# Kernel optimization log

Hardware: AMD Instinct MI355X
Metric: run time of the kernel (lower is better)

Reference implementation:

```python
import jax, jax.numpy as jnp
import numpy as np

B, T, D, H = 4, 2048, 1024, 16
HD = D // H  # head_dim = 64
ROPE_BASE = 10000.0


def rotate_half(x):
    # Faithful to source: interleaved rotate. x[..., ::2], x[..., 1::2]
    x1 = x[..., ::2]
    x2 = x[..., 1::2]
    return jnp.stack((-x2, x1), axis=-1).reshape(x.shape)


def rope_tables(seq_len, dim, dtype=jnp.float32):
    inv = 1.0 / (ROPE_BASE ** (jnp.arange(0, dim, 2, dtype=jnp.float32) / dim))
    t = jnp.arange(seq_len, dtype=jnp.float32)
    freqs = jnp.einsum('i,j->ij', t, inv)          # [T, dim/2]
    emb = jnp.concatenate((freqs, freqs), axis=-1)  # [T, dim]
    return jnp.cos(emb).astype(dtype)[None, None], jnp.sin(emb).astype(dtype)[None, None]


def setup_inputs() -> dict:
    key = jax.random.key(0)
    ks = jax.random.split(key, 9)
    s = 0.02
    return {
        'x':  jax.random.normal(ks[0], (B, T, D), jnp.float32),
        'Wq': jax.random.normal(ks[1], (D, D), jnp.float32) * s,
        'bq': jnp.zeros((D,), jnp.float32),
        'Wk': jax.random.normal(ks[2], (D, D), jnp.float32) * s,
        'bk': jnp.zeros((D,), jnp.float32),
        'Wv': jax.random.normal(ks[3], (D, D), jnp.float32) * s,
        'bv': jnp.zeros((D,), jnp.float32),
        'Wo': jax.random.normal(ks[4], (D, D), jnp.float32) * s,
        'bo': jnp.zeros((D,), jnp.float32),
    }


def reference(x, Wq, bq, Wk, bk, Wv, bv, Wo, bo):
    b, t, d = x.shape
    # QKV projections -> [B, H, T, HD]
    def proj(W, bias):
        return (x @ W.T + bias).reshape(b, t, H, HD).transpose(0, 2, 1, 3)
    q, k, v = proj(Wq, bq), proj(Wk, bk), proj(Wv, bv)
    # RoPE (as written in source: non-interleaved cos/sin with interleaved rotate_half)
    cos, sin = rope_tables(t, HD, x.dtype)
    q = q * cos + rotate_half(q) * sin
    k = k * cos + rotate_half(k) * sin
    # Attention
    scale = 1.0 / jnp.sqrt(jnp.asarray(HD, x.dtype))
    attn = jnp.einsum('bhqd,bhkd->bhqk', q, k) * scale
    attn = jax.nn.softmax(attn, axis=-1)
    out = jnp.einsum('bhqk,bhkd->bhqd', attn, v)
    out = out.transpose(0, 2, 1, 3).reshape(b, t, d)
    return out @ Wo.T + bo
```

## Files before the change

### kernel.cpp

```cpp
#include <hip/hip_runtime.h>
#include <hip/hip_bf16.h>

constexpr int Bb = 4, Tt = 2048, Dd = 1024, Hh = 16, HD = 64;
constexpr int Mm = Bb * Tt;

typedef __attribute__((ext_vector_type(8))) short bf16x8;
typedef __attribute__((ext_vector_type(4))) short s16x4;
typedef __attribute__((ext_vector_type(4))) float f32x4;
typedef __attribute__((ext_vector_type(16))) float f32x16;

__device__ __forceinline__ short f2bf(float f) {
  union { float f; unsigned u; } v; v.f = f;
  unsigned r = (v.u + 0x7fffu + ((v.u >> 16) & 1u)) >> 16;
  return (short)r;
}

__device__ __forceinline__ unsigned cvt_pk_bf16(float lo, float hi) {
  unsigned r;
  asm("v_cvt_pk_bf16_f32 %0, %1, %2" : "=v"(r) : "v"(lo), "v"(hi));
  return r;
}

__device__ __forceinline__ void gl_lds16(const short* gsrc, short* ldst) {
  __builtin_amdgcn_global_load_lds(
      (const __attribute__((address_space(1))) void*)gsrc,
      (__attribute__((address_space(3))) void*)ldst, 16, 0, 0);
}

__global__ __launch_bounds__(256) void cvt_k(const float* __restrict__ src,
                                             short* __restrict__ dst, int n4) {
  int i = blockIdx.x * 256 + threadIdx.x;
  if (i >= n4) return;
  float4 v = ((const float4*)src)[i];
  s16x4 p = { f2bf(v.x), f2bf(v.y), f2bf(v.z), f2bf(v.w) };
  ((s16x4*)dst)[i] = p;
}

__global__ void rope_tab(float* __restrict__ cs, float* __restrict__ sn) {
  int idx = blockIdx.x * 256 + threadIdx.x;
  if (idx >= Tt * HD) return;
  int t = idx >> 6, d = idx & (HD - 1);
  float f = powf(10000.0f, -(float)(d & 31) / 32.0f);
  float ang = (float)t * f;
  cs[idx] = cosf(ang);
  sn[idx] = sinf(ang);
}

template<int EPI>
__global__ __launch_bounds__(256) void gemm_fast(
    const short* __restrict__ Ab, const short* __restrict__ Wb,
    const float* __restrict__ bias,
    short* __restrict__ outb, float* __restrict__ outf,
    const float* __restrict__ cs, const float* __restrict__ sn)
{
  constexpr int K = 1024;
  __shared__ short Alds[128 * 64];
  __shared__ short Blds[128 * 64];
  const int tid = threadIdx.x;
  const int lane = tid & 63, wave = tid >> 6;
  const int g = lane >> 4, li = lane & 15;
  const int m0 = blockIdx.x * 128, n0 = blockIdx.y * 128;
  const int wm = (wave >> 1) * 64, wn = (wave & 1) * 64;
  f32x4 acc[4][4] = {};

  const int lrow = lane >> 3;
  const int soff = lrow * K + (((lane & 7) ^ lrow) * 8);
  const short* Asrc = Ab + (size_t)(m0 + wave * 32) * K + soff;
  const short* Bsrc = Wb + (size_t)(n0 + wave * 32) * K + soff;
  short* Adst = Alds + wave * 32 * 64;
  short* Bdst = Blds + wave * 32 * 64;

  for (int k0 = 0; k0 < K; k0 += 64) {
    #pragma unroll
    for (int i = 0; i < 4; i++) {
      gl_lds16(Asrc + (size_t)i * 8 * K + k0, Adst + i * 8 * 64);
      gl_lds16(Bsrc + (size_t)i * 8 * K + k0, Bdst + i * 8 * 64);
    }
    __syncthreads();

    bf16x8 af[4][2], bfr[4][2];
    #pragma unroll
    for (int i = 0; i < 4; i++) {
      int row = wm + i * 16 + li, sw = li & 7;
      #pragma unroll
      for (int kk = 0; kk < 2; kk++)
        af[i][kk] = *(const bf16x8*)&Alds[row * 64 + (((kk * 4 + g) ^ sw) * 8)];
    }
    #pragma unroll
    for (int j = 0; j < 4; j++) {
      int row = wn + j * 16 + li, sw = li & 7;
      #pragma unroll
      for (int kk = 0; kk < 2; kk++)
        bfr[j][kk] = *(const bf16x8*)&Blds[row * 64 + (((kk * 4 + g) ^ sw) * 8)];
    }
    #pragma unroll
    for (int i = 0; i < 4; i++)
      #pragma unroll
      for (int j = 0; j < 4; j++)
        #pragma unroll
        for (int kk = 0; kk < 2; kk++)
          acc[i][j] = __builtin_amdgcn_mfma_f32_16x16x32_bf16(
              af[i][kk], bfr[j][kk], acc[i][j], 0, 0, 0);
    __syncthreads();
  }

  #pragma unroll
  for (int i = 0; i < 4; i++)
    #pragma unroll
    for (int j = 0; j < 4; j++)
      #pragma unroll
      for (int r = 0; r < 4; r++) {
        int m = m0 + wm + i * 16 + g * 4 + r;
        int n = n0 + wn + j * 16 + li;
        float val = acc[i][j][r] + bias[n];
        if constexpr (EPI == 0 || EPI == 1) {
          float partner = __shfl_xor(val, 1, 64);
          int tt = m & (Tt - 1), hd = n & (HD - 1);
          float c = cs[tt * HD + hd], s = sn[tt * HD + hd];
          float rh = (n & 1) ? partner : -partner;
          val = val * c + rh * s;
          if constexpr (EPI == 0) val *= 0.18033688f;
        }
        if constexpr (EPI <= 1) {
          int bI = m >> 11, tt = m & (Tt - 1), h = n >> 6, hd = n & (HD - 1);
          outb[(((size_t)bI * Hh + h) * Tt + tt) * HD + hd] = f2bf(val);
        } else {
          outf[(size_t)m * Dd + n] = val;
        }
      }
}

__global__ __launch_bounds__(256) void gemm_v(
    const short* __restrict__ Ab, const float* __restrict__ Wf,
    const float* __restrict__ bias, short* __restrict__ outb)
{
  constexpr int K = 1024;
  __shared__ short Alds[128][72];
  __shared__ short Blds[128][72];
  const int tid = threadIdx.x;
  const int lane = tid & 63, wave = tid >> 6;
  const int g = lane >> 4, li = lane & 15;
  const int m0 = blockIdx.x * 128, n0 = blockIdx.y * 128;
  const int wm = (wave >> 1) * 64, wn = (wave & 1) * 64;
  f32x4 acc[4][4] = {};

  for (int k0 = 0; k0 < K; k0 += 64) {
    #pragma unroll
    for (int s = 0; s < 4; s++) {
      int f = tid + s * 256; int row = f >> 3, c8 = f & 7;
      *(bf16x8*)&Alds[row][c8 * 8] =
          *(const bf16x8*)(Ab + (size_t)(m0 + row) * K + k0 + c8 * 8);
    }
    #pragma unroll
    for (int s = 0; s < 8; s++) {
      int f = tid + s * 256; int row = f >> 4, c4 = f & 15;
      float4 v = *(const float4*)(Wf + (size_t)(n0 + row) * K + k0 + c4 * 4);
      s16x4 p = { f2bf(v.x), f2bf(v.y), f2bf(v.z), f2bf(v.w) };
      *(s16x4*)&Blds[row][c4 * 4] = p;
    }
    __syncthreads();

    bf16x8 af[4][2], bfr[4][2];
    #pragma unroll
    for (int i = 0; i < 4; i++)
      #pragma unroll
      for (int kk = 0; kk < 2; kk++)
        af[i][kk] = *(const bf16x8*)&Alds[wm + i * 16 + li][kk * 32 + g * 8];
    #pragma unroll
    for (int j = 0; j < 4; j++)
      #pragma unroll
      for (int kk = 0; kk < 2; kk++)
        bfr[j][kk] = *(const bf16x8*)&Blds[wn + j * 16 + li][kk * 32 + g * 8];
    #pragma unroll
    for (int i = 0; i < 4; i++)
      #pragma unroll
      for (int j = 0; j < 4; j++)
        #pragma unroll
        for (int kk = 0; kk < 2; kk++)
          acc[i][j] = __builtin_amdgcn_mfma_f32_16x16x32_bf16(
              af[i][kk], bfr[j][kk], acc[i][j], 0, 0, 0);
    __syncthreads();
  }

  #pragma unroll
  for (int i = 0; i < 4; i++)
    #pragma unroll
    for (int j = 0; j < 4; j++) {
      int n = n0 + wn + j * 16 + li;
      s16x4 pk;
      #pragma unroll
      for (int r = 0; r < 4; r++) pk[r] = f2bf(acc[i][j][r] + bias[n]);
      int mb = m0 + wm + i * 16 + g * 4;
      int bI = mb >> 11, t0 = mb & (Tt - 1), h = n >> 6, d = n & (HD - 1);
      *(s16x4*)(outb + (((size_t)bI * Hh + h) * HD + d) * Tt + t0) = pk;
    }
}

__device__ __forceinline__ void store_o(const f32x16& o, float inv,
                                        short* __restrict__ AO, size_t rowbase,
                                        int colbase, int h) {
  #pragma unroll
  for (int R = 0; R < 4; R++) {
    s16x4 pk;
    #pragma unroll
    for (int j = 0; j < 4; j++) pk[j] = f2bf(o[R * 4 + j] * inv);
    *(s16x4*)(AO + rowbase + colbase + 8 * R + 4 * h) = pk;
  }
}

__global__ __launch_bounds__(128, 4) void attn_k(
    const short* __restrict__ Qb, const short* __restrict__ Kb,
    const short* __restrict__ Vt_g, short* __restrict__ AO)
{
  __shared__ short Klds[64][72];
  __shared__ short Vt[64][72];
  const int tid = threadIdx.x, lane = tid & 63, wave = tid >> 6;
  const int h = lane >> 5;
  const int ql = lane & 31;
  const int bh = blockIdx.x;
  const int q0 = blockIdx.y * 64 + wave * 32;
  const size_t base  = (size_t)bh * Tt * HD;
  const size_t basev = (size_t)bh * HD * Tt;

  bf16x8 qf[4];
  #pragma unroll
  for (int ks = 0; ks < 4; ks++)
    qf[ks] = *(const bf16x8*)(Qb + base + (size_t)(q0 + ql) * HD + ks * 16 + h * 8);

  float m_i = -3.0e38f, l_i = 0.f;
  f32x16 o0 = {}, o1 = {};

  for (int kv0 = 0; kv0 < Tt; kv0 += 64) {
    #pragma unroll
    for (int s = 0; s < 4; s++) {
      int f = tid + s * 128; int row = f >> 3, c8 = f & 7;
      *(bf16x8*)&Klds[row][c8 * 8] =
          *(const bf16x8*)(Kb + base + (size_t)(kv0 + row) * HD + c8 * 8);
      *(bf16x8*)&Vt[row][c8 * 8] =
          *(const bf16x8*)(Vt_g + basev + (size_t)row * Tt + kv0 + c8 * 8);
    }
    __syncthreads();

    f32x16 st0 = {}, st1 = {};
    __builtin_amdgcn_s_setprio(1);
    #pragma unroll
    for (int ks = 0; ks < 4; ks++) {
      bf16x8 kf0 = *(const bf16x8*)&Klds[ql][ks * 16 + h * 8];
      bf16x8 kf1 = *(const bf16x8*)&Klds[32 + ql][ks * 16 + h * 8];
      st0 = __builtin_amdgcn_mfma_f32_32x32x16_bf16(kf0, qf[ks], st0, 0, 0, 0);
      st1 = __builtin_amdgcn_mfma_f32_32x32x16_bf16(kf1, qf[ks], st1, 0, 0, 0);
    }
    __builtin_amdgcn_s_setprio(0);

    float mv = st0[0];
    #pragma unroll
    for (int r = 1; r < 16; r++) mv = fmaxf(mv, st0[r]);
    #pragma unroll
    for (int r = 0; r < 16; r++) mv = fmaxf(mv, st1[r]);
    mv = fmaxf(mv, __shfl_xor(mv, 32, 64));
    float mn = fmaxf(m_i, mv);
    float corr = __builtin_amdgcn_exp2f(m_i - mn);
    m_i = mn;

    float rs = 0.f;
    #pragma unroll
    for (int r = 0; r < 16; r++) { st0[r] = __builtin_amdgcn_exp2f(st0[r] - mn); rs += st0[r]; }
    #pragma unroll
    for (int r = 0; r < 16; r++) { st1[r] = __builtin_amdgcn_exp2f(st1[r] - mn); rs += st1[r]; }
    rs += __shfl_xor(rs, 32, 64);
    l_i = l_i * corr + rs;

    #pragma unroll
    for (int r = 0; r < 16; r++) { o0[r] *= corr; o1[r] *= corr; }

    __builtin_amdgcn_s_setprio(1);
    #pragma unroll
    for (int ks = 0; ks < 4; ks++) {
      const int b0 = ((2 * ks) & 3) * 4;
      float A0, A1, A2, A3, B0, B1, B2, B3;
      if (ks < 2) {
        A0 = st0[b0]; A1 = st0[b0 + 1]; A2 = st0[b0 + 2]; A3 = st0[b0 + 3];
        B0 = st0[b0 + 4]; B1 = st0[b0 + 5]; B2 = st0[b0 + 6]; B3 = st0[b0 + 7];
      } else {
        A0 = st1[b0]; A1 = st1[b0 + 1]; A2 = st1[b0 + 2]; A3 = st1[b0 + 3];
        B0 = st1[b0 + 4]; B1 = st1[b0 + 5]; B2 = st1[b0 + 6]; B3 = st1[b0 + 7];
      }
      unsigned wa0 = cvt_pk_bf16(A0, A1), wa1 = cvt_pk_bf16(A2, A3);
      unsigned wb0 = cvt_pk_bf16(B0, B1), wb1 = cvt_pk_bf16(B2, B3);
      unsigned s0 = h ? wa0 : wb0, s1 = h ? wa1 : wb1;
      unsigned r0 = (unsigned)__shfl_xor((int)s0, 32, 64);
      unsigned r1 = (unsigned)__shfl_xor((int)s1, 32, 64);
      unsigned own0 = h ? wb0 : wa0, own1 = h ? wb1 : wa1;
      union { unsigned u[4]; bf16x8 v; } pa;
      pa.u[0] = h ? r0 : own0;  pa.u[1] = h ? r1 : own1;
      pa.u[2] = h ? own0 : r0;  pa.u[3] = h ? own1 : r1;

      bf16x8 vf0 = *(const bf16x8*)&Vt[ql][ks * 16 + h * 8];
      bf16x8 vf1 = *(const bf16x8*)&Vt[32 + ql][ks * 16 + h * 8];
      o0 = __builtin_amdgcn_mfma_f32_32x32x16_bf16(vf0, pa.v, o0, 0, 0, 0);
      o1 = __builtin_amdgcn_mfma_f32_32x32x16_bf16(vf1, pa.v, o1, 0, 0, 0);
    }
    __builtin_amdgcn_s_setprio(0);
    __syncthreads();
  }

  float inv = 1.0f / l_i;
  const int b = bh >> 4, hh = bh & 15;
  size_t rowbase = ((size_t)b * Tt + q0 + ql) * Dd;
  store_o(o0, inv, AO, rowbase, hh * 64 + 0, h);
  store_o(o1, inv, AO, rowbase, hh * 64 + 32, h);
}

extern "C" void kernel_launch(void* const* d_in, const int* in_sizes, int n_in,
                              void* d_out, int out_size, void* d_ws, size_t ws_size,
                              hipStream_t stream)
{
  const float* x  = (const float*)d_in[0];
  const float* Wq = (const float*)d_in[1];
  const float* bq = (const float*)d_in[2];
  const float* Wk = (const float*)d_in[3];
  const float* bk = (const float*)d_in[4];
  const float* Wv = (const float*)d_in[5];
  const float* bv = (const float*)d_in[6];
  const float* Wo = (const float*)d_in[7];
  const float* bo = (const float*)d_in[8];
  float* out = (float*)d_out;

  char* ws = (char*)d_ws;
  float* cs = (float*)ws;
  float* sn = (float*)(ws + (size_t)(1 << 19));
  char*  p0 = ws + ((size_t)1 << 20);
  short* Qb = (short*)(p0);
  short* Kb = (short*)(p0 + ((size_t)16 << 20));
  short* Vb = (short*)(p0 + ((size_t)32 << 20));
  short* xb = (short*)(p0 + ((size_t)48 << 20));
  short* AO  = xb;
  short* Wqb = Kb;
  short* Wkb = Vb;
  short* Wob = Kb;

  cvt_k<<<dim3(Mm * Dd / 4 / 256), dim3(256), 0, stream>>>(x,  xb,  Mm * Dd / 4);
  cvt_k<<<dim3(Dd * Dd / 4 / 256), dim3(256), 0, stream>>>(Wq, Wqb, Dd * Dd / 4);
  cvt_k<<<dim3(Dd * Dd / 4 / 256), dim3(256), 0, stream>>>(Wk, Wkb, Dd * Dd / 4);
  rope_tab<<<dim3(512), dim3(256), 0, stream>>>(cs, sn);

  dim3 gg(Mm / 128, Dd / 128), bb(256);
  gemm_fast<0><<<gg, bb, 0, stream>>>(xb, Wqb, bq, Qb, nullptr, cs, sn);
  gemm_fast<1><<<gg, bb, 0, stream>>>(xb, Wkb, bk, Kb, nullptr, cs, sn);
  gemm_v<<<gg, bb, 0, stream>>>(xb, Wv, bv, Vb);

  attn_k<<<dim3(Bb * Hh, Tt / 64), dim3(128), 0, stream>>>(Qb, Kb, Vb, AO);

  cvt_k<<<dim3(Dd * Dd / 4 / 256), dim3(256), 0, stream>>>(Wo, Wob, Dd * Dd / 4);
  gemm_fast<3><<<gg, bb, 0, stream>>>(AO, Wob, bo, nullptr, out, cs, sn);
}
```

Measured before the change: 232.6 us.

## Batch Q/K projections into one launch and add lazy softmax rescaling

Merges the Q and K projection GEMMs into a single launch that picks the weight, bias and output by blockIdx.z, moving the weight buffers so both converted weights can live at once. The separate output-projection GEMM kernel is specialised to drop the RoPE epilogue branches. In attention, the row max now uses a v_max3 reduction tree, and the running max and rescale of the output and sum are only updated when the new max exceeds the old one by more than 8 in log2 space. Skipping the rescale removes per-tile multiplies but lets exponentials reach up to 2^8 before normalisation, which slightly changes the numerics.

```diff
diff --git a/kernel.cpp b/kernel.cpp
--- a/kernel.cpp
+++ b/kernel.cpp
@@ -19,6 +19,12 @@
   unsigned r;
   asm("v_cvt_pk_bf16_f32 %0, %1, %2" : "=v"(r) : "v"(lo), "v"(hi));
   return r;
+}
+
+__device__ __forceinline__ float max3f(float a, float b, float c) {
+  float d;
+  asm("v_max3_f32 %0, %1, %2, %3" : "=v"(d) : "v"(a), "v"(b), "v"(c));
+  return d;
 }
 
 __device__ __forceinline__ void gl_lds16(const short* gsrc, short* ldst) {
@@ -46,12 +52,92 @@
   sn[idx] = sinf(ang);
 }
 
-template<int EPI>
-__global__ __launch_bounds__(256) void gemm_fast(
+__global__ __launch_bounds__(256) void gemm_qk(
+    const short* __restrict__ Ab,
+    const short* __restrict__ Wqb, const short* __restrict__ Wkb,
+    const float* __restrict__ bq, const float* __restrict__ bk,
+    short* __restrict__ Qo, short* __restrict__ Ko,
+    const float* __restrict__ cs, const float* __restrict__ sn)
+{
+  constexpr int K = 1024;
+  __shared__ short Alds[128 * 64];
+  __shared__ short Blds[128 * 64];
+  const bool isQ = (blockIdx.z == 0);
+  const short* Wb = isQ ? Wqb : Wkb;
+  const float* bias = isQ ? bq : bk;
+  short* outb = isQ ? Qo : Ko;
+  const float scale = isQ ? 0.18033688f : 1.0f;
+
+  const int tid = threadIdx.x;
+  const int lane = tid & 63, wave = tid >> 6;
+  const int g = lane >> 4, li = lane & 15;
+  const int m0 = blockIdx.x * 128, n0 = blockIdx.y * 128;
+  const int wm = (wave >> 1) * 64, wn = (wave & 1) * 64;
+  f32x4 acc[4][4] = {};
+
+  const int lrow = lane >> 3;
+  const int soff = lrow * K + (((lane & 7) ^ lrow) * 8);
+  const short* Asrc = Ab + (size_t)(m0 + wave * 32) * K + soff;
+  const short* Bsrc = Wb + (size_t)(n0 + wave * 32) * K + soff;
+  short* Adst = Alds + wave * 32 * 64;
+  short* Bdst = Blds + wave * 32 * 64;
+
+  for (int k0 = 0; k0 < K; k0 += 64) {
+    #pragma unroll
+    for (int i = 0; i < 4; i++) {
+      gl_lds16(Asrc + (size_t)i * 8 * K + k0, Adst + i * 8 * 64);
+      gl_lds16(Bsrc + (size_t)i * 8 * K + k0, Bdst + i * 8 * 64);
+    }
+    __syncthreads();
+
+    bf16x8 af[4][2], bfr[4][2];
+    #pragma unroll
+    for (int i = 0; i < 4; i++) {
+      int row = wm + i * 16 + li, sw = li & 7;
+      #pragma unroll
+      for (int kk = 0; kk < 2; kk++)
+        af[i][kk] = *(const bf16x8*)&Alds[row * 64 + (((kk * 4 + g) ^ sw) * 8)];
+    }
+    #pragma unroll
+    for (int j = 0; j < 4; j++) {
+      int row = wn + j * 16 + li, sw = li & 7;
+      #pragma unroll
+      for (int kk = 0; kk < 2; kk++)
+        bfr[j][kk] = *(const bf16x8*)&Blds[row * 64 + (((kk * 4 + g) ^ sw) * 8)];
+    }
+    #pragma unroll
+    for (int i = 0; i < 4; i++)
+      #pragma unroll
+      for (int j = 0; j < 4; j++)
+        #pragma unroll
+        for (int kk = 0; kk < 2; kk++)
+          acc[i][j] = __builtin_amdgcn_mfma_f32_16x16x32_bf16(
+              af[i][kk], bfr[j][kk], acc[i][j], 0, 0, 0);
+    __syncthreads();
+  }
+
+  #pragma unroll
+  for (int i = 0; i < 4; i++)
+    #pragma unroll
+    for (int j = 0; j < 4; j++)
+      #pragma unroll
+      for (int r = 0; r < 4; r++) {
+        int m = m0 + wm + i * 16 + g * 4 + r;
+        int n = n0 + wn + j * 16 + li;
+        float val = acc[i][j][r] + bias[n];
+        float partner = __shfl_xor(val, 1, 64);
+        int tt = m & (Tt - 1), hd = n & (HD - 1);
+        float c = cs[tt * HD + hd], s = sn[tt * HD + hd];
+        float rh = (n & 1) ? partner : -partner;
+        val = (val * c + rh * s) * scale;
+        int bI = m >> 11, h = n >> 6;
+        outb[(((size_t)bI * Hh + h) * Tt + tt) * HD + hd] = f2bf(val);
+      }
+}
+
+__global__ __launch_bounds__(256) void gemm_fin(
     const short* __restrict__ Ab, const short* __restrict__ Wb,
-    const float* __restrict__ bias,
-    short* __restrict__ outb, float* __restrict__ outf,
-    const float* __restrict__ cs, const float* __restrict__ sn)
+    const float* __restrict__ bias, float* __restrict__ outf)
 {
   constexpr int K = 1024;
   __shared__ short Alds[128 * 64];
@@ -112,21 +198,7 @@
       for (int r = 0; r < 4; r++) {
         int m = m0 + wm + i * 16 + g * 4 + r;
         int n = n0 + wn + j * 16 + li;
-        float val = acc[i][j][r] + bias[n];
-        if constexpr (EPI == 0 || EPI == 1) {
-          float partner = __shfl_xor(val, 1, 64);
-          int tt = m & (Tt - 1), hd = n & (HD - 1);
-          float c = cs[tt * HD + hd], s = sn[tt * HD + hd];
-          float rh = (n & 1) ? partner : -partner;
-          val = val * c + rh * s;
-          if constexpr (EPI == 0) val *= 0.18033688f;
-        }
-        if constexpr (EPI <= 1) {
-          int bI = m >> 11, tt = m & (Tt - 1), h = n >> 6, hd = n & (HD - 1);
-          outb[(((size_t)bI * Hh + h) * Tt + tt) * HD + hd] = f2bf(val);
-        } else {
-          outf[(size_t)m * Dd + n] = val;
-        }
+        outf[(size_t)m * Dd + n] = acc[i][j][r] + bias[n];
       }
 }
 
@@ -252,26 +324,40 @@
     }
     __builtin_amdgcn_s_setprio(0);
 
-    float mv = st0[0];
-    #pragma unroll
-    for (int r = 1; r < 16; r++) mv = fmaxf(mv, st0[r]);
-    #pragma unroll
-    for (int r = 0; r < 16; r++) mv = fmaxf(mv, st1[r]);
+    float t0 = max3f(st0[0],  st0[1],  st0[2]);
+    float t1 = max3f(st0[3],  st0[4],  st0[5]);
+    float t2 = max3f(st0[6],  st0[7],  st0[8]);
+    float t3 = max3f(st0[9],  st0[10], st0[11]);
+    float t4 = max3f(st0[12], st0[13], st0[14]);
+    float t5 = max3f(st0[15], st1[0],  st1[1]);
+    float t6 = max3f(st1[2],  st1[3],  st1[4]);
+    float t7 = max3f(st1[5],  st1[6],  st1[7]);
+    float t8 = max3f(st1[8],  st1[9],  st1[10]);
+    float t9 = max3f(st1[11], st1[12], st1[13]);
+    float ta = fmaxf(st1[14], st1[15]);
+    float u0 = max3f(t0, t1, t2);
+    float u1 = max3f(t3, t4, t5);
+    float u2 = max3f(t6, t7, t8);
+    float u3 = fmaxf(t9, ta);
+    float mv = fmaxf(max3f(u0, u1, u2), u3);
     mv = fmaxf(mv, __shfl_xor(mv, 32, 64));
-    float mn = fmaxf(m_i, mv);
-    float corr = __builtin_amdgcn_exp2f(m_i - mn);
-    m_i = mn;
+
+    if (!__all(mv <= m_i + 8.0f)) {
+      float mn = fmaxf(m_i, mv);
+      float corr = __builtin_amdgcn_exp2f(m_i - mn);
+      m_i = mn;
+      l_i *= corr;
+      #pragma unroll
+      for (int r = 0; r < 16; r++) { o0[r] *= corr; o1[r] *= corr; }
+    }
 
     float rs = 0.f;
     #pragma unroll
-    for (int r = 0; r < 16; r++) { st0[r] = __builtin_amdgcn_exp2f(st0[r] - mn); rs += st0[r]; }
-    #pragma unroll
-    for (int r = 0; r < 16; r++) { st1[r] = __builtin_amdgcn_exp2f(st1[r] - mn); rs += st1[r]; }
+    for (int r = 0; r < 16; r++) { st0[r] = __builtin_amdgcn_exp2f(st0[r] - m_i); rs += st0[r]; }
+    #pragma unroll
+    for (int r = 0; r < 16; r++) { st1[r] = __builtin_amdgcn_exp2f(st1[r] - m_i); rs += st1[r]; }
     rs += __shfl_xor(rs, 32, 64);
-    l_i = l_i * corr + rs;
-
-    #pragma unroll
-    for (int r = 0; r < 16; r++) { o0[r] *= corr; o1[r] *= corr; }
+    l_i += rs;
 
     __builtin_amdgcn_s_setprio(1);
     #pragma unroll
@@ -335,8 +421,8 @@
   short* Vb = (short*)(p0 + ((size_t)32 << 20));
   short* xb = (short*)(p0 + ((size_t)48 << 20));
   short* AO  = xb;
-  short* Wqb = Kb;
-  short* Wkb = Vb;
+  short* Wqb = Vb;
+  short* Wkb = (short*)(p0 + ((size_t)34 << 20));
   short* Wob = Kb;
 
   cvt_k<<<dim3(Mm * Dd / 4 / 256), dim3(256), 0, stream>>>(x,  xb,  Mm * Dd / 4);
@@ -344,13 +430,13 @@
   cvt_k<<<dim3(Dd * Dd / 4 / 256), dim3(256), 0, stream>>>(Wk, Wkb, Dd * Dd / 4);
   rope_tab<<<dim3(512), dim3(256), 0, stream>>>(cs, sn);
 
-  dim3 gg(Mm / 128, Dd / 128), bb(256);
-  gemm_fast<0><<<gg, bb, 0, stream>>>(xb, Wqb, bq, Qb, nullptr, cs, sn);
-  gemm_fast<1><<<gg, bb, 0, stream>>>(xb, Wkb, bk, Kb, nullptr, cs, sn);
-  gemm_v<<<gg, bb, 0, stream>>>(xb, Wv, bv, Vb);
+  dim3 bb(256);
+  gemm_qk<<<dim3(Mm / 128, Dd / 128, 2), bb, 0, stream>>>(
+      xb, Wqb, Wkb, bq, bk, Qb, Kb, cs, sn);
+  gemm_v<<<dim3(Mm / 128, Dd / 128), bb, 0, stream>>>(xb, Wv, bv, Vb);
 
   attn_k<<<dim3(Bb * Hh, Tt / 64), dim3(128), 0, stream>>>(Qb, Kb, Vb, AO);
 
   cvt_k<<<dim3(Dd * Dd / 4 / 256), dim3(256), 0, stream>>>(Wo, Wob, Dd * Dd / 4);
-  gemm_fast<3><<<gg, bb, 0, stream>>>(AO, Wob, bo, nullptr, out, cs, sn);
-}
+  gemm_fin<<<dim3(Mm / 128, Dd / 128), bb, 0, stream>>>(AO, Wob, bo, out);
+}
```

New measurement: 224.4 us. 1.04x faster.
